# Kernel optimization log

Hardware: AMD Instinct MI355X
Metric: run time of the kernel (lower is better)

Reference implementation:

```python
import jax, jax.numpy as jnp
import numpy as np


def _mlp2(x, W1, b1, W2, b2):
    # ReluMLP with two Dense layers: relu between layers, linear output
    return jax.nn.relu(x @ W1 + b1) @ W2 + b2


def setup_inputs() -> dict:
    key = jax.random.key(0)
    N, NP, DIN, D = 100000, 25000, 16, 64
    E, EDS, EP, EUS = 1_600_000, 800_000, 400_000, 200_000
    L = 8  # number of message-passing layers actually used
    ks = iter(jax.random.split(key, 40))
    nrm = lambda shape: jax.random.normal(next(ks), shape, jnp.float32) * 0.05
    ri = lambda n, hi: jax.random.randint(next(ks), (n,), 0, hi)
    return dict(
        x=jax.random.normal(next(ks), (N, DIN), jnp.float32),
        We1=nrm((DIN, D)), be1=jnp.zeros((D,), jnp.float32),
        We2=nrm((D, D)), be2=jnp.zeros((D,), jnp.float32),
        Wm1=nrm((L, D, D)), bm1=jnp.zeros((L, D), jnp.float32),
        Wm2=nrm((L, D, D)), bm2=jnp.zeros((L, D), jnp.float32),
        Wn1=nrm((L, 2 * D, D)), bn1=jnp.zeros((L, D), jnp.float32),
        Wn2=nrm((L, D, D)), bn2=jnp.zeros((L, D), jnp.float32),
        Wd1=nrm((D, D)), bd1=jnp.zeros((D,), jnp.float32),
        Wd2=nrm((D, 2)), bd2=jnp.zeros((2,), jnp.float32),
        s_fine=ri(E, N), r_fine=ri(E, N),
        s_ds=ri(EDS, N), r_ds=ri(EDS, N),
        s_p=ri(EP, NP), r_p=ri(EP, NP),
        s_us=ri(EUS, NP), r_us=ri(EUS, NP),
        uppool=ri(N, NP), downpool=ri(NP, NP),
    )


def reference(x, We1, be1, We2, be2, Wm1, bm1, Wm2, bm2, Wn1, bn1, Wn2, bn2,
              Wd1, bd1, Wd2, bd2, s_fine, r_fine, s_ds, r_ds, s_p, r_p,
              s_us, r_us, uppool, downpool):
    def mp(l, h, s, r, n):
        # LinearMessagePassingLayer: message MLP on sender feats,
        # sum-scatter to receivers (mean_aggr=False), node MLP on [h, aggr]
        msg = _mlp2(h[s], Wm1[l], bm1[l], Wm2[l], bm2[l])          # [E, D]
        aggr = jax.ops.segment_sum(msg, r, num_segments=n)          # [n, D]
        return _mlp2(jnp.concatenate([h, aggr], -1),
                     Wn1[l], bn1[l], Wn2[l], bn2[l])                # [n, D]

    N = x.shape[0]
    NP = downpool.shape[0]
    # encode
    h = _mlp2(x, We1, be1, We2, be2)                                 # [N, D]
    h = mp(0, h, s_fine, r_fine, N)
    h = mp(1, h, s_fine, r_fine, N)
    skip = h
    # Downsample: gather by uppool idx, MP on downsampling graph, select pooled
    g = mp(2, h[uppool], s_ds, r_ds, N)                              # [N, D]
    hp = g[downpool]                                                 # [NP, D]
    # bottleneck
    hp = mp(3, hp, s_p, r_p, NP)
    hp = mp(4, hp, s_p, r_p, NP)
    # Upsample: gather by downpool idx, MP on upsampling graph, select by uppool
    g = mp(5, hp[downpool], s_us, r_us, NP)                          # [NP, D]
    h = g[uppool]                                                    # [N, D]
    # decode with skip connections
    h = mp(6, h, s_fine, r_fine, N) + skip
    h = mp(7, h, s_fine, r_fine, N) + skip
    return _mlp2(h, Wd1, bd1, Wd2, bd2)                              # [N, 2]
```

## Files before the change

kernel.cpp:

```cpp
#include <hip/hip_runtime.h>

#define WG 256

#define MLP_FMA16(ACC, A, W) do { \
    ACC[0][0]=fmaf(A.x,W.x,ACC[0][0]); ACC[0][1]=fmaf(A.x,W.y,ACC[0][1]); \
    ACC[0][2]=fmaf(A.x,W.z,ACC[0][2]); ACC[0][3]=fmaf(A.x,W.w,ACC[0][3]); \
    ACC[1][0]=fmaf(A.y,W.x,ACC[1][0]); ACC[1][1]=fmaf(A.y,W.y,ACC[1][1]); \
    ACC[1][2]=fmaf(A.y,W.z,ACC[1][2]); ACC[1][3]=fmaf(A.y,W.w,ACC[1][3]); \
    ACC[2][0]=fmaf(A.z,W.x,ACC[2][0]); ACC[2][1]=fmaf(A.z,W.y,ACC[2][1]); \
    ACC[2][2]=fmaf(A.z,W.z,ACC[2][2]); ACC[2][3]=fmaf(A.z,W.w,ACC[2][3]); \
    ACC[3][0]=fmaf(A.w,W.x,ACC[3][0]); ACC[3][1]=fmaf(A.w,W.y,ACC[3][1]); \
    ACC[3][2]=fmaf(A.w,W.z,ACC[3][2]); ACC[3][3]=fmaf(A.w,W.w,ACC[3][3]); \
} while (0)

__device__ __forceinline__ void fill_role(int xcd, int w,
    const int* __restrict__ s, const int* __restrict__ r,
    int* __restrict__ cur, int* __restrict__ sl,
    int cap, int E, int n, int W)
{
    const int lo = (int)(((long)n * xcd) >> 3);
    const int hi = (int)(((long)n * (xcd + 1)) >> 3);
    int chunk = (E + W - 1) / W;
    chunk = (chunk + 3) & ~3;
    const int e0 = w * chunk;
    const int e1 = min(E, e0 + chunk);

    auto fill1 = [&](int v, int e) {
        if (v >= lo && v < hi) {
            const int sv = s[e];
            const int p = atomicAdd(&cur[v], 1);
            if (p < cap) sl[(size_t)v * cap + p] = sv;
        }
    };

    for (int e = e0 + (int)threadIdx.x * 4; e < e1; e += WG * 4) {
        if (e + 4 <= e1) {
            const int4 rv = *(const int4*)&r[e];
            fill1(rv.x, e + 0);
            fill1(rv.y, e + 1);
            fill1(rv.z, e + 2);
            fill1(rv.w, e + 3);
        } else {
            for (int j = 0; e + j < e1; ++j) fill1(r[e + j], e + j);
        }
    }
}

struct FillPair {
    const int* s0; const int* r0; int* cur0; int* sl0; int cap0, E0, n0, W0;
    const int* s1; const int* r1; int* cur1; int* sl1; int cap1, E1, n1, W1;
    int FILLB;
};

template<int DINA, bool HAS_B, bool HAS_SKIP, bool GATHER_A,
         int MSG_DOUT, bool PARTIAL_MSG, bool WRITE_OUT1>
__global__ __launch_bounds__(WG)
void mlp2_fused(const float* __restrict__ inA, const int* __restrict__ gidxA,
                const float* __restrict__ inB,
                const float* __restrict__ W1, const float* __restrict__ b1,
                const float* __restrict__ W2, const float* __restrict__ b2,
                const float* __restrict__ skip, float* __restrict__ out1,
                const float* __restrict__ M1, const float* __restrict__ mb1,
                const float* __restrict__ M2, const float* __restrict__ mb2,
                float* __restrict__ outM, int msgN, int n, FillPair fa)
{
    if (fa.FILLB > 0 && (int)blockIdx.x < fa.FILLB) {
        const int xcd = blockIdx.x & 7;
        const int w = blockIdx.x >> 3;
        if (w < fa.W0)
            fill_role(xcd, w, fa.s0, fa.r0, fa.cur0, fa.sl0, fa.cap0, fa.E0, fa.n0, fa.W0);
        else
            fill_role(xcd, w - fa.W0, fa.s1, fa.r1, fa.cur1, fa.sl1, fa.cap1, fa.E1, fa.n1, fa.W1);
        return;
    }
    const int bid = blockIdx.x - fa.FILLB;

    constexpr int XP = 68;
    __shared__ __align__(16) float sXT[64][XP];
    __shared__ __align__(16) float sW[64 * 64];
    __shared__ float sb[128];
    __shared__ float sW2d[128];
    __shared__ float sb2d[2];

    const int tid = threadIdx.x;
    const int tx = tid & 15, ty = tid >> 4;
    const int c0 = tx * 4, r0 = ty * 4;
    const int row0 = bid * 64;
    const int lrow = tid & 63;
    const int kq0 = (tid >> 6) * 4;

    for (int i = tid * 4; i < DINA * 64; i += WG * 4)
        *(float4*)&sW[i] = *(const float4*)&W1[i];
    if (tid < 64) sb[tid] = b1[tid];
    else if (tid < 128) sb[tid] = b2[tid - 64];

    {
        const int rg = min(row0 + lrow, n - 1);
        const int ra = GATHER_A ? gidxA[rg] : rg;
        const float* pA = inA + (size_t)ra * DINA;
        #pragma unroll
        for (int kq = kq0; kq < DINA; kq += 16) {
            const float4 v = *(const float4*)(pA + kq);
            sXT[kq + 0][lrow] = v.x; sXT[kq + 1][lrow] = v.y;
            sXT[kq + 2][lrow] = v.z; sXT[kq + 3][lrow] = v.w;
        }
    }
    __syncthreads();

    float acc[4][4] = {};
    #pragma unroll 8
    for (int k = 0; k < DINA; ++k) {
        const float4 a = *(const float4*)&sXT[k][r0];
        const float4 w = *(const float4*)&sW[k * 64 + c0];
        MLP_FMA16(acc, a, w);
    }

    if constexpr (HAS_B) {
        __syncthreads();
        for (int i = tid * 4; i < 64 * 64; i += WG * 4)
            *(float4*)&sW[i] = *(const float4*)&W1[DINA * 64 + i];
        {
            const int rg = min(row0 + lrow, n - 1);
            const float* pB = inB + (size_t)rg * 64;
            #pragma unroll
            for (int kq = kq0; kq < 64; kq += 16) {
                const float4 v = *(const float4*)(pB + kq);
                sXT[kq + 0][lrow] = v.x; sXT[kq + 1][lrow] = v.y;
                sXT[kq + 2][lrow] = v.z; sXT[kq + 3][lrow] = v.w;
            }
        }
        __syncthreads();
        #pragma unroll 8
        for (int k = 0; k < 64; ++k) {
            const float4 a = *(const float4*)&sXT[k][r0];
            const float4 w = *(const float4*)&sW[k * 64 + c0];
            MLP_FMA16(acc, a, w);
        }
    }
    __syncthreads();

    for (int i = tid * 4; i < 64 * 64; i += WG * 4)
        *(float4*)&sW[i] = *(const float4*)&W2[i];
    #pragma unroll
    for (int j = 0; j < 4; ++j) {
        const float bj = sb[c0 + j];
        *(float4*)&sXT[c0 + j][r0] = make_float4(
            fmaxf(acc[0][j] + bj, 0.f), fmaxf(acc[1][j] + bj, 0.f),
            fmaxf(acc[2][j] + bj, 0.f), fmaxf(acc[3][j] + bj, 0.f));
    }
    __syncthreads();

    float acc2[4][4] = {};
    #pragma unroll 8
    for (int k = 0; k < 64; ++k) {
        const float4 a = *(const float4*)&sXT[k][r0];
        const float4 w = *(const float4*)&sW[k * 64 + c0];
        MLP_FMA16(acc2, a, w);
    }

    float ofull[4][4];
    #pragma unroll
    for (int i = 0; i < 4; ++i) {
        const int row = row0 + r0 + i;
        float4 s = make_float4(0.f, 0.f, 0.f, 0.f);
        if (HAS_SKIP && row < n) s = *(const float4*)&skip[(size_t)row * 64 + c0];
        ofull[i][0] = acc2[i][0] + sb[64 + c0 + 0] + s.x;
        ofull[i][1] = acc2[i][1] + sb[64 + c0 + 1] + s.y;
        ofull[i][2] = acc2[i][2] + sb[64 + c0 + 2] + s.z;
        ofull[i][3] = acc2[i][3] + sb[64 + c0 + 3] + s.w;
        if (WRITE_OUT1 && row < n)
            *(float4*)&out1[(size_t)row * 64 + c0] =
                make_float4(ofull[i][0], ofull[i][1], ofull[i][2], ofull[i][3]);
    }

    if constexpr (MSG_DOUT > 0) {
        if (!PARTIAL_MSG || row0 < msgN) {
            __syncthreads();
            for (int i = tid * 4; i < 64 * 64; i += WG * 4)
                *(float4*)&sW[i] = *(const float4*)&M1[i];
            if constexpr (MSG_DOUT == 64) {
                if (tid < 64) sb[tid] = mb1[tid];
                else if (tid < 128) sb[tid] = mb2[tid - 64];
            } else {
                if (tid < 64) sb[tid] = mb1[tid];
                else if (tid < 192) sW2d[tid - 64] = M2[tid - 64];
                else if (tid < 194) sb2d[tid - 192] = mb2[tid - 192];
            }
            #pragma unroll
            for (int j = 0; j < 4; ++j)
                *(float4*)&sXT[c0 + j][r0] =
                    make_float4(ofull[0][j], ofull[1][j], ofull[2][j], ofull[3][j]);
            __syncthreads();

            float acc3[4][4] = {};
            #pragma unroll 8
            for (int k = 0; k < 64; ++k) {
                const float4 a = *(const float4*)&sXT[k][r0];
                const float4 w = *(const float4*)&sW[k * 64 + c0];
                MLP_FMA16(acc3, a, w);
            }
            __syncthreads();
            if constexpr (MSG_DOUT == 64) {
                for (int i = tid * 4; i < 64 * 64; i += WG * 4)
                    *(float4*)&sW[i] = *(const float4*)&M2[i];
            }
            #pragma unroll
            for (int j = 0; j < 4; ++j) {
                const float bj = sb[c0 + j];
                *(float4*)&sXT[c0 + j][r0] = make_float4(
                    fmaxf(acc3[0][j] + bj, 0.f), fmaxf(acc3[1][j] + bj, 0.f),
                    fmaxf(acc3[2][j] + bj, 0.f), fmaxf(acc3[3][j] + bj, 0.f));
            }
            __syncthreads();

            if constexpr (MSG_DOUT == 64) {
                float accM[4][4] = {};
                #pragma unroll 8
                for (int k = 0; k < 64; ++k) {
                    const float4 a = *(const float4*)&sXT[k][r0];
                    const float4 w = *(const float4*)&sW[k * 64 + c0];
                    MLP_FMA16(accM, a, w);
                }
                #pragma unroll
                for (int i = 0; i < 4; ++i) {
                    const int row = row0 + r0 + i;
                    if (row < msgN)
                        *(float4*)&outM[(size_t)row * 64 + c0] =
                            make_float4(accM[i][0] + sb[64 + c0 + 0],
                                        accM[i][1] + sb[64 + c0 + 1],
                                        accM[i][2] + sb[64 + c0 + 2],
                                        accM[i][3] + sb[64 + c0 + 3]);
                }
            } else {
                if (tid < 128) {
                    const int lr = tid >> 1, col = tid & 1;
                    float o0 = sb2d[col], o1 = 0.0f;
                    #pragma unroll 8
                    for (int k = 0; k < 64; k += 2) {
                        o0 = fmaf(sXT[k][lr],     sW2d[k * 2 + col],       o0);
                        o1 = fmaf(sXT[k + 1][lr], sW2d[(k + 1) * 2 + col], o1);
                    }
                    const int row = row0 + lr;
                    if (row < msgN) outM[(size_t)row * 2 + col] = o0 + o1;
                }
            }
        }
    }
}

template<int DINA, bool HAS_B, bool HAS_SKIP, bool GATHER_A>
__global__ __launch_bounds__(WG)
void mlp2_rt(const float* __restrict__ inA, const int* __restrict__ gidxA,
             const float* __restrict__ inB,
             const float* __restrict__ W1, const float* __restrict__ b1,
             const float* __restrict__ W2, const float* __restrict__ b2,
             const float* __restrict__ skip,
             float* __restrict__ out, int n)
{
    constexpr int XP = 68;
    __shared__ __align__(16) float sXT[64][XP];
    __shared__ __align__(16) float sW[64 * 64];
    __shared__ float sb[128];

    const int tid = threadIdx.x;
    const int tx = tid & 15, ty = tid >> 4;
    const int c0 = tx * 4, r0 = ty * 4;
    const int row0 = blockIdx.x * 64;
    const int lrow = tid & 63;
    const int kq0 = (tid >> 6) * 4;

    for (int i = tid * 4; i < DINA * 64; i += WG * 4)
        *(float4*)&sW[i] = *(const float4*)&W1[i];
    if (tid < 64) sb[tid] = b1[tid];
    else if (tid < 128) sb[tid] = b2[tid - 64];

    {
        const int rg = min(row0 + lrow, n - 1);
        const int ra = GATHER_A ? gidxA[rg] : rg;
        const float* pA = inA + (size_t)ra * DINA;
        #pragma unroll
        for (int kq = kq0; kq < DINA; kq += 16) {
            const float4 v = *(const float4*)(pA + kq);
            sXT[kq + 0][lrow] = v.x; sXT[kq + 1][lrow] = v.y;
            sXT[kq + 2][lrow] = v.z; sXT[kq + 3][lrow] = v.w;
        }
    }
    __syncthreads();

    float acc[4][4] = {};
    #pragma unroll 8
    for (int k = 0; k < DINA; ++k) {
        const float4 a = *(const float4*)&sXT[k][r0];
        const float4 w = *(const float4*)&sW[k * 64 + c0];
        MLP_FMA16(acc, a, w);
    }
    if constexpr (HAS_B) {
        __syncthreads();
        for (int i = tid * 4; i < 64 * 64; i += WG * 4)
            *(float4*)&sW[i] = *(const float4*)&W1[DINA * 64 + i];
        {
            const int rg = min(row0 + lrow, n - 1);
            const float* pB = inB + (size_t)rg * 64;
            #pragma unroll
            for (int kq = kq0; kq < 64; kq += 16) {
                const float4 v = *(const float4*)(pB + kq);
                sXT[kq + 0][lrow] = v.x; sXT[kq + 1][lrow] = v.y;
                sXT[kq + 2][lrow] = v.z; sXT[kq + 3][lrow] = v.w;
            }
        }
        __syncthreads();
        #pragma unroll 8
        for (int k = 0; k < 64; ++k) {
            const float4 a = *(const float4*)&sXT[k][r0];
            const float4 w = *(const float4*)&sW[k * 64 + c0];
            MLP_FMA16(acc, a, w);
        }
    }
    __syncthreads();

    for (int i = tid * 4; i < 64 * 64; i += WG * 4)
        *(float4*)&sW[i] = *(const float4*)&W2[i];
    #pragma unroll
    for (int j = 0; j < 4; ++j) {
        const float bj = sb[c0 + j];
        *(float4*)&sXT[c0 + j][r0] = make_float4(
            fmaxf(acc[0][j] + bj, 0.f), fmaxf(acc[1][j] + bj, 0.f),
            fmaxf(acc[2][j] + bj, 0.f), fmaxf(acc[3][j] + bj, 0.f));
    }
    __syncthreads();

    float acc2[4][4] = {};
    #pragma unroll 8
    for (int k = 0; k < 64; ++k) {
        const float4 a = *(const float4*)&sXT[k][r0];
        const float4 w = *(const float4*)&sW[k * 64 + c0];
        MLP_FMA16(acc2, a, w);
    }
    #pragma unroll
    for (int i = 0; i < 4; ++i) {
        const int row = row0 + r0 + i;
        if (row < n) {
            float4 o = make_float4(acc2[i][0] + sb[64 + c0 + 0],
                                   acc2[i][1] + sb[64 + c0 + 1],
                                   acc2[i][2] + sb[64 + c0 + 2],
                                   acc2[i][3] + sb[64 + c0 + 3]);
            if (HAS_SKIP) {
                const float4 s = *(const float4*)&skip[(size_t)row * 64 + c0];
                o.x += s.x; o.y += s.y; o.z += s.z; o.w += s.w;
            }
            *(float4*)&out[(size_t)row * 64 + c0] = o;
        }
    }
}

__global__ __launch_bounds__(WG)
void fill_enc_k(const int* __restrict__ s0, const int* __restrict__ r0v,
                int* cu0, int* sl0, int cap0, int E0, int n0, int W0, int FILLB,
                const float* __restrict__ x,
                const float* __restrict__ We1, const float* __restrict__ be1,
                const float* __restrict__ We2, const float* __restrict__ be2,
                float* __restrict__ h0,
                const float* __restrict__ M1, const float* __restrict__ mb1,
                const float* __restrict__ M2, const float* __restrict__ mb2,
                float* __restrict__ msg0, int N)
{
    constexpr int XP = 68;
    __shared__ __align__(16) float sXT[64][XP];
    __shared__ float sb[128];

    if ((int)blockIdx.x < FILLB) {
        fill_role(blockIdx.x & 7, blockIdx.x >> 3, s0, r0v, cu0, sl0, cap0, E0, n0, W0);
        return;
    }

    const int bid = blockIdx.x - FILLB;
    const int tid = threadIdx.x;
    const int tx = tid & 15, ty = tid >> 4;
    const int c0 = tx * 4, r0 = ty * 4;
    const int row0 = bid * 64;
    const int lrow = tid & 63;
    const int kq0 = (tid >> 6) * 4;

    if (tid < 64) sb[tid] = be1[tid];
    else if (tid < 128) sb[tid] = be2[tid - 64];

    {
        const int rg = min(row0 + lrow, N - 1);
        const float* pA = x + (size_t)rg * 16;
        const float4 v = *(const float4*)(pA + kq0);
        sXT[kq0 + 0][lrow] = v.x; sXT[kq0 + 1][lrow] = v.y;
        sXT[kq0 + 2][lrow] = v.z; sXT[kq0 + 3][lrow] = v.w;
    }
    __syncthreads();

    float acc[4][4] = {};
    #pragma unroll
    for (int k = 0; k < 16; ++k) {
        const float4 a = *(const float4*)&sXT[k][r0];
        const float4 w = *(const float4*)&We1[k * 64 + c0];
        MLP_FMA16(acc, a, w);
    }
    __syncthreads();
    #pragma unroll
    for (int j = 0; j < 4; ++j) {
        const float bj = sb[c0 + j];
        *(float4*)&sXT[c0 + j][r0] = make_float4(
            fmaxf(acc[0][j] + bj, 0.f), fmaxf(acc[1][j] + bj, 0.f),
            fmaxf(acc[2][j] + bj, 0.f), fmaxf(acc[3][j] + bj, 0.f));
    }
    __syncthreads();

    float acc2[4][4] = {};
    #pragma unroll 8
    for (int k = 0; k < 64; ++k) {
        const float4 a = *(const float4*)&sXT[k][r0];
        const float4 w = *(const float4*)&We2[k * 64 + c0];
        MLP_FMA16(acc2, a, w);
    }
    float ofull[4][4];
    #pragma unroll
    for (int i = 0; i < 4; ++i) {
        const int row = row0 + r0 + i;
        ofull[i][0] = acc2[i][0] + sb[64 + c0 + 0];
        ofull[i][1] = acc2[i][1] + sb[64 + c0 + 1];
        ofull[i][2] = acc2[i][2] + sb[64 + c0 + 2];
        ofull[i][3] = acc2[i][3] + sb[64 + c0 + 3];
        if (row < N)
            *(float4*)&h0[(size_t)row * 64 + c0] =
                make_float4(ofull[i][0], ofull[i][1], ofull[i][2], ofull[i][3]);
    }

    __syncthreads();
    if (tid < 64) sb[tid] = mb1[tid];
    else if (tid < 128) sb[tid] = mb2[tid - 64];
    #pragma unroll
    for (int j = 0; j < 4; ++j)
        *(float4*)&sXT[c0 + j][r0] =
            make_float4(ofull[0][j], ofull[1][j], ofull[2][j], ofull[3][j]);
    __syncthreads();

    float acc3[4][4] = {};
    #pragma unroll 8
    for (int k = 0; k < 64; ++k) {
        const float4 a = *(const float4*)&sXT[k][r0];
        const float4 w = *(const float4*)&M1[k * 64 + c0];
        MLP_FMA16(acc3, a, w);
    }
    __syncthreads();
    #pragma unroll
    for (int j = 0; j < 4; ++j) {
        const float bj = sb[c0 + j];
        *(float4*)&sXT[c0 + j][r0] = make_float4(
            fmaxf(acc3[0][j] + bj, 0.f), fmaxf(acc3[1][j] + bj, 0.f),
            fmaxf(acc3[2][j] + bj, 0.f), fmaxf(acc3[3][j] + bj, 0.f));
    }
    __syncthreads();

    float accM[4][4] = {};
    #pragma unroll 8
    for (int k = 0; k < 64; ++k) {
        const float4 a = *(const float4*)&sXT[k][r0];
        const float4 w = *(const float4*)&M2[k * 64 + c0];
        MLP_FMA16(accM, a, w);
    }
    #pragma unroll
    for (int i = 0; i < 4; ++i) {
        const int row = row0 + r0 + i;
        if (row < N)
            *(float4*)&msg0[(size_t)row * 64 + c0] =
                make_float4(accM[i][0] + sb[64 + c0 + 0],
                            accM[i][1] + sb[64 + c0 + 1],
                            accM[i][2] + sb[64 + c0 + 2],
                            accM[i][3] + sb[64 + c0 + 3]);
    }
}

template<bool REMAP>
__global__ __launch_bounds__(WG)
void gather_slots_k(const int* __restrict__ deg, const int* __restrict__ slots,
                    int cap, const int* __restrict__ remap,
                    const float* __restrict__ tab, float* __restrict__ aggr, int n)
{
    const int node = blockIdx.x * (WG / 64) + (threadIdx.x >> 6);
    const int c = threadIdx.x & 63;
    if (node >= n) return;
    const int d = min(deg[node], cap);
    const int* sl = slots + (size_t)node * cap;

    int myidx = 0;
    if (c < d) {
        myidx = sl[c];
        if (REMAP) myidx = remap[myidx];
    }

    float a[8] = {};
    int j = 0;
    for (; j + 7 < d; j += 8) {
        #pragma unroll
        for (int u = 0; u < 8; ++u) {
            const int t = __shfl(myidx, j + u);
            a[u] += tab[(size_t)t * 64 + c];
        }
    }
    #pragma unroll 4
    for (; j < d; ++j) {
        const int t = __shfl(myidx, j);
        a[j & 7] += tab[(size_t)t * 64 + c];
    }
    aggr[(size_t)node * 64 + c] =
        ((a[0] + a[1]) + (a[2] + a[3])) + ((a[4] + a[5]) + (a[6] + a[7]));
}

extern "C" void kernel_launch(void* const* d_in, const int* in_sizes, int n_in,
                              void* d_out, int out_size, void* d_ws, size_t ws_size,
                              hipStream_t stream)
{
    const float* x    = (const float*)d_in[0];
    const float* We1  = (const float*)d_in[1];
    const float* be1  = (const float*)d_in[2];
    const float* We2  = (const float*)d_in[3];
    const float* be2  = (const float*)d_in[4];
    const float* Wm1  = (const float*)d_in[5];
    const float* bm1  = (const float*)d_in[6];
    const float* Wm2  = (const float*)d_in[7];
    const float* bm2  = (const float*)d_in[8];
    const float* Wn1  = (const float*)d_in[9];
    const float* bn1  = (const float*)d_in[10];
    const float* Wn2  = (const float*)d_in[11];
    const float* bn2  = (const float*)d_in[12];
    const float* Wd1  = (const float*)d_in[13];
    const float* bd1  = (const float*)d_in[14];
    const float* Wd2  = (const float*)d_in[15];
    const float* bd2  = (const float*)d_in[16];
    const int* s_fine = (const int*)d_in[17];
    const int* r_fine = (const int*)d_in[18];
    const int* s_ds   = (const int*)d_in[19];
    const int* r_ds   = (const int*)d_in[20];
    const int* s_p    = (const int*)d_in[21];
    const int* r_p    = (const int*)d_in[22];
    const int* s_us   = (const int*)d_in[23];
    const int* r_us   = (const int*)d_in[24];
    const int* uppool   = (const int*)d_in[25];
    const int* downpool = (const int*)d_in[26];

    const int N   = in_sizes[0] / 16;
    const int E   = in_sizes[17];
    const int EDS = in_sizes[19];
    const int EP  = in_sizes[21];
    const int EUS = in_sizes[23];
    const int NP  = in_sizes[26];

    const int CAP_FINE = 48, CAP_DS = 32, CAP_PP = 48, CAP_US = 32;

    float* B0  = (float*)d_ws;
    float* B1  = B0 + (size_t)N * 64;
    float* B2  = B1 + (size_t)N * 64;
    float* B3  = B2 + (size_t)N * 64;
    float* HPa = B3 + (size_t)N * 64;
    float* HPb = HPa + (size_t)NP * 64;
    int* ip = (int*)(HPb + (size_t)NP * 64);
    auto alloc_i = [&](size_t n) { int* p = ip; ip += n; return p; };
    int* cur_fine = alloc_i(N);
    int* cur_ds   = alloc_i(N);
    int* cur_pp   = alloc_i(NP);
    int* cur_us   = alloc_i(NP);
    int* sl_fine  = alloc_i((size_t)N * CAP_FINE);
    int* sl_ds    = alloc_i((size_t)N * CAP_DS);
    int* sl_pp    = alloc_i((size_t)NP * CAP_PP);
    int* sl_us    = alloc_i((size_t)NP * CAP_US);

    const int gN  = (N + 63) / 64;
    const int gNP = (NP + 63) / 64;
    const int gaN  = (N + 3) / 4;
    const int gaNP = (NP + 3) / 4;

    const FillPair fnone = {};

    hipMemsetAsync(cur_fine, 0, (size_t)(2 * N + 2 * NP) * sizeof(int), stream);
    {
        const int W_FINE = 256;
        const int FILLB = 8 * W_FINE;
        fill_enc_k<<<FILLB + gN, WG, 0, stream>>>(
            s_fine, r_fine, cur_fine, sl_fine, CAP_FINE, E, N, W_FINE, FILLB,
            x, We1, be1, We2, be2, B0,
            Wm1 + 0*4096, bm1 + 0*64, Wm2 + 0*4096, bm2 + 0*64, B1, N);
    }
    gather_slots_k<false><<<gaN,WG,0,stream>>>(cur_fine,sl_fine,CAP_FINE,nullptr,B1,B2,N);

    {
        const int W_DS = 128;
        FillPair fds = { s_ds, r_ds, cur_ds, sl_ds, CAP_DS, EDS, N, W_DS,
                         nullptr, nullptr, nullptr, nullptr, 0, 0, 0, 0,
                         8 * W_DS };
        mlp2_fused<64,true,false,false,64,false,true><<<8*W_DS + gN,WG,0,stream>>>(
            B0,nullptr,B2, Wn1+0*8192,bn1+0*64,Wn2+0*4096,bn2+0*64, nullptr,B3,
            Wm1+1*4096,bm1+1*64,Wm2+1*4096,bm2+1*64, B0, N, N, fds);
    }
    gather_slots_k<false><<<gaN,WG,0,stream>>>(cur_fine,sl_fine,CAP_FINE,nullptr,B0,B2,N);

    {
        const int W_PP = 64, W_US = 32;
        FillPair fpu = { s_p,  r_p,  cur_pp, sl_pp, CAP_PP, EP,  NP, W_PP,
                         s_us, r_us, cur_us, sl_us, CAP_US, EUS, NP, W_US,
                         8 * (W_PP + W_US) };
        mlp2_fused<64,true,false,false,64,true,true><<<8*(W_PP+W_US) + gN,WG,0,stream>>>(
            B3,nullptr,B2, Wn1+1*8192,bn1+1*64,Wn2+1*4096,bn2+1*64, nullptr,B1,
            Wm1+2*4096,bm1+2*64,Wm2+2*4096,bm2+2*64, B0, NP, N, fpu);
    }
    gather_slots_k<true><<<gaN,WG,0,stream>>>(cur_ds,sl_ds,CAP_DS,uppool,B0,B2,N);

    mlp2_rt<64,true,false,true><<<gN,WG,0,stream>>>(
        B1,uppool,B2, Wn1+2*8192,bn1+2*64,Wn2+2*4096,bn2+2*64, nullptr,B3,N);

    mlp2_rt<64,false,false,true><<<gNP,WG,0,stream>>>(
        B3,downpool,nullptr, Wm1+3*4096,bm1+3*64,Wm2+3*4096,bm2+3*64, nullptr,HPa,NP);
    gather_slots_k<false><<<gaNP,WG,0,stream>>>(cur_pp,sl_pp,CAP_PP,nullptr,HPa,B2,NP);

    mlp2_fused<64,true,false,true,64,false,true><<<gNP,WG,0,stream>>>(
        B3,downpool,B2, Wn1+3*8192,bn1+3*64,Wn2+3*4096,bn2+3*64, nullptr,HPb,
        Wm1+4*4096,bm1+4*64,Wm2+4*4096,bm2+4*64, HPa, NP, NP, fnone);
    gather_slots_k<false><<<gaNP,WG,0,stream>>>(cur_pp,sl_pp,CAP_PP,nullptr,HPa,B2,NP);

    mlp2_fused<64,true,false,false,64,false,true><<<gNP,WG,0,stream>>>(
        HPb,nullptr,B2, Wn1+4*8192,bn1+4*64,Wn2+4*4096,bn2+4*64, nullptr,HPa,
        Wm1+5*4096,bm1+5*64,Wm2+5*4096,bm2+5*64, HPb, NP, NP, fnone);
    gather_slots_k<true><<<gaNP,WG,0,stream>>>(cur_us,sl_us,CAP_US,downpool,HPb,B2,NP);

    mlp2_fused<64,true,false,true,64,false,true><<<gNP,WG,0,stream>>>(
        HPa,downpool,B2, Wn1+5*8192,bn1+5*64,Wn2+5*4096,bn2+5*64, nullptr,HPb,
        Wm1+6*4096,bm1+6*64,Wm2+6*4096,bm2+6*64, B3, NP, NP, fnone);
    gather_slots_k<true><<<gaN,WG,0,stream>>>(cur_fine,sl_fine,CAP_FINE,uppool,B3,B2,N);

    mlp2_fused<64,true,true,true,64,false,true><<<gN,WG,0,stream>>>(
        HPb,uppool,B2, Wn1+6*8192,bn1+6*64,Wn2+6*4096,bn2+6*64, B1,B0,
        Wm1+7*4096,bm1+7*64,Wm2+7*4096,bm2+7*64, B3, N, N, fnone);
    gather_slots_k<false><<<gaN,WG,0,stream>>>(cur_fine,sl_fine,CAP_FINE,nullptr,B3,B2,N);

    mlp2_fused<64,true,true,false,2,false,false><<<gN,WG,0,stream>>>(
        B0,nullptr,B2, Wn1+7*8192,bn1+7*64,Wn2+7*4096,bn2+7*64, B1,nullptr,
        Wd1,bd1,Wd2,bd2, (float*)d_out, N, N, fnone);
}
```

Before: 988.1 us.

## Fuse slot-based neighbor aggregation into node-MLP kernels, removing gather launches

Removes the standalone gather_slots_k kernels. The per-receiver sum over CSR-like slots now runs inside the node-MLP kernel and writes straight into shared memory. This avoids writing and re-reading the [n,64] aggregate buffer and cuts roughly eight launches. In exchange, each block's wavefronts walk 16 nodes serially, with variable degree inside the MLP kernel. That can hurt latency hiding and occupancy, and the layer-7 message MLP is split out into its own launch.

```diff
diff --git a/kernel.cpp b/kernel.cpp
--- a/kernel.cpp
+++ b/kernel.cpp
@@ -1,6 +1,7 @@
 #include <hip/hip_runtime.h>
 
 #define WG 256
+constexpr int XP = 68;
 
 #define MLP_FMA16(ACC, A, W) do { \
     ACC[0][0]=fmaf(A.x,W.x,ACC[0][0]); ACC[0][1]=fmaf(A.x,W.y,ACC[0][1]); \
@@ -52,17 +53,58 @@
     int FILLB;
 };
 
-template<int DINA, bool HAS_B, bool HAS_SKIP, bool GATHER_A,
+template<bool REMAP>
+__device__ __forceinline__ void gather_stage(
+    float (*sXT)[XP], int row0, int n,
+    const int* __restrict__ deg, const int* __restrict__ slots, int cap,
+    const int* __restrict__ remap, const float* __restrict__ tab, int tid)
+{
+    const int lane = tid & 63;
+    const int wv = tid >> 6;
+    #pragma unroll 1
+    for (int nn = 0; nn < 16; ++nn) {
+        const int ndl = wv * 16 + nn;
+        const int nd = row0 + ndl;
+        int d = 0;
+        const int* sl = slots;
+        if (nd < n) { d = min(deg[nd], cap); sl = slots + (size_t)nd * cap; }
+        int myidx = 0;
+        if (lane < d) {
+            myidx = sl[lane];
+            if (REMAP) myidx = remap[myidx];
+        }
+        float a[8] = {};
+        int j = 0;
+        for (; j + 7 < d; j += 8) {
+            #pragma unroll
+            for (int u = 0; u < 8; ++u) {
+                const int t = __shfl(myidx, j + u);
+                a[u] += tab[(size_t)t * 64 + lane];
+            }
+        }
+        #pragma unroll 4
+        for (; j < d; ++j) {
+            const int t = __shfl(myidx, j);
+            a[j & 7] += tab[(size_t)t * 64 + lane];
+        }
+        sXT[lane][ndl] =
+            ((a[0] + a[1]) + (a[2] + a[3])) + ((a[4] + a[5]) + (a[6] + a[7]));
+    }
+}
+
+template<int DINA, bool HAS_B, bool HAS_SKIP, bool GATHER_A, bool REMAP_B,
          int MSG_DOUT, bool PARTIAL_MSG, bool WRITE_OUT1>
 __global__ __launch_bounds__(WG)
 void mlp2_fused(const float* __restrict__ inA, const int* __restrict__ gidxA,
-                const float* __restrict__ inB,
                 const float* __restrict__ W1, const float* __restrict__ b1,
                 const float* __restrict__ W2, const float* __restrict__ b2,
                 const float* __restrict__ skip, float* __restrict__ out1,
                 const float* __restrict__ M1, const float* __restrict__ mb1,
                 const float* __restrict__ M2, const float* __restrict__ mb2,
-                float* __restrict__ outM, int msgN, int n, FillPair fa)
+                float* __restrict__ outM, int msgN, int n,
+                const int* __restrict__ degB, const int* __restrict__ slotsB,
+                int capB, const int* __restrict__ remapB,
+                const float* __restrict__ tabB, FillPair fa)
 {
     if (fa.FILLB > 0 && (int)blockIdx.x < fa.FILLB) {
         const int xcd = blockIdx.x & 7;
@@ -75,7 +117,6 @@
     }
     const int bid = blockIdx.x - fa.FILLB;
 
-    constexpr int XP = 68;
     __shared__ __align__(16) float sXT[64][XP];
     __shared__ __align__(16) float sW[64 * 64];
     __shared__ float sb[128];
@@ -119,16 +160,7 @@
         __syncthreads();
         for (int i = tid * 4; i < 64 * 64; i += WG * 4)
             *(float4*)&sW[i] = *(const float4*)&W1[DINA * 64 + i];
-        {
-            const int rg = min(row0 + lrow, n - 1);
-            const float* pB = inB + (size_t)rg * 64;
-            #pragma unroll
-            for (int kq = kq0; kq < 64; kq += 16) {
-                const float4 v = *(const float4*)(pB + kq);
-                sXT[kq + 0][lrow] = v.x; sXT[kq + 1][lrow] = v.y;
-                sXT[kq + 2][lrow] = v.z; sXT[kq + 3][lrow] = v.w;
-            }
-        }
+        gather_stage<REMAP_B>(sXT, row0, n, degB, slotsB, capB, remapB, tabB, tid);
         __syncthreads();
         #pragma unroll 8
         for (int k = 0; k < 64; ++k) {
@@ -248,111 +280,6 @@
     }
 }
 
-template<int DINA, bool HAS_B, bool HAS_SKIP, bool GATHER_A>
-__global__ __launch_bounds__(WG)
-void mlp2_rt(const float* __restrict__ inA, const int* __restrict__ gidxA,
-             const float* __restrict__ inB,
-             const float* __restrict__ W1, const float* __restrict__ b1,
-             const float* __restrict__ W2, const float* __restrict__ b2,
-             const float* __restrict__ skip,
-             float* __restrict__ out, int n)
-{
-    constexpr int XP = 68;
-    __shared__ __align__(16) float sXT[64][XP];
-    __shared__ __align__(16) float sW[64 * 64];
-    __shared__ float sb[128];
-
-    const int tid = threadIdx.x;
-    const int tx = tid & 15, ty = tid >> 4;
-    const int c0 = tx * 4, r0 = ty * 4;
-    const int row0 = blockIdx.x * 64;
-    const int lrow = tid & 63;
-    const int kq0 = (tid >> 6) * 4;
-
-    for (int i = tid * 4; i < DINA * 64; i += WG * 4)
-        *(float4*)&sW[i] = *(const float4*)&W1[i];
-    if (tid < 64) sb[tid] = b1[tid];
-    else if (tid < 128) sb[tid] = b2[tid - 64];
-
-    {
-        const int rg = min(row0 + lrow, n - 1);
-        const int ra = GATHER_A ? gidxA[rg] : rg;
-        const float* pA = inA + (size_t)ra * DINA;
-        #pragma unroll
-        for (int kq = kq0; kq < DINA; kq += 16) {
-            const float4 v = *(const float4*)(pA + kq);
-            sXT[kq + 0][lrow] = v.x; sXT[kq + 1][lrow] = v.y;
-            sXT[kq + 2][lrow] = v.z; sXT[kq + 3][lrow] = v.w;
-        }
-    }
-    __syncthreads();
-
-    float acc[4][4] = {};
-    #pragma unroll 8
-    for (int k = 0; k < DINA; ++k) {
-        const float4 a = *(const float4*)&sXT[k][r0];
-        const float4 w = *(const float4*)&sW[k * 64 + c0];
-        MLP_FMA16(acc, a, w);
-    }
-    if constexpr (HAS_B) {
-        __syncthreads();
-        for (int i = tid * 4; i < 64 * 64; i += WG * 4)
-            *(float4*)&sW[i] = *(const float4*)&W1[DINA * 64 + i];
-        {
-            const int rg = min(row0 + lrow, n - 1);
-            const float* pB = inB + (size_t)rg * 64;
-            #pragma unroll
-            for (int kq = kq0; kq < 64; kq += 16) {
-                const float4 v = *(const float4*)(pB + kq);
-                sXT[kq + 0][lrow] = v.x; sXT[kq + 1][lrow] = v.y;
-                sXT[kq + 2][lrow] = v.z; sXT[kq + 3][lrow] = v.w;
-            }
-        }
-        __syncthreads();
-        #pragma unroll 8
-        for (int k = 0; k < 64; ++k) {
-            const float4 a = *(const float4*)&sXT[k][r0];
-            const float4 w = *(const float4*)&sW[k * 64 + c0];
-            MLP_FMA16(acc, a, w);
-        }
-    }
-    __syncthreads();
-
-    for (int i = tid * 4; i < 64 * 64; i += WG * 4)
-        *(float4*)&sW[i] = *(const float4*)&W2[i];
-    #pragma unroll
-    for (int j = 0; j < 4; ++j) {
-        const float bj = sb[c0 + j];
-        *(float4*)&sXT[c0 + j][r0] = make_float4(
-            fmaxf(acc[0][j] + bj, 0.f), fmaxf(acc[1][j] + bj, 0.f),
-            fmaxf(acc[2][j] + bj, 0.f), fmaxf(acc[3][j] + bj, 0.f));
-    }
-    __syncthreads();
-
-    float acc2[4][4] = {};
-    #pragma unroll 8
-    for (int k = 0; k < 64; ++k) {
-        const float4 a = *(const float4*)&sXT[k][r0];
-        const float4 w = *(const float4*)&sW[k * 64 + c0];
-        MLP_FMA16(acc2, a, w);
-    }
-    #pragma unroll
-    for (int i = 0; i < 4; ++i) {
-        const int row = row0 + r0 + i;
-        if (row < n) {
-            float4 o = make_float4(acc2[i][0] + sb[64 + c0 + 0],
-                                   acc2[i][1] + sb[64 + c0 + 1],
-                                   acc2[i][2] + sb[64 + c0 + 2],
-                                   acc2[i][3] + sb[64 + c0 + 3]);
-            if (HAS_SKIP) {
-                const float4 s = *(const float4*)&skip[(size_t)row * 64 + c0];
-                o.x += s.x; o.y += s.y; o.z += s.z; o.w += s.w;
-            }
-            *(float4*)&out[(size_t)row * 64 + c0] = o;
-        }
-    }
-}
-
 __global__ __launch_bounds__(WG)
 void fill_enc_k(const int* __restrict__ s0, const int* __restrict__ r0v,
                 int* cu0, int* sl0, int cap0, int E0, int n0, int W0, int FILLB,
@@ -364,7 +291,6 @@
                 const float* __restrict__ M2, const float* __restrict__ mb2,
                 float* __restrict__ msg0, int N)
 {
-    constexpr int XP = 68;
     __shared__ __align__(16) float sXT[64][XP];
     __shared__ float sb[128];
 
@@ -473,42 +399,6 @@
                             accM[i][2] + sb[64 + c0 + 2],
                             accM[i][3] + sb[64 + c0 + 3]);
     }
-}
-
-template<bool REMAP>
-__global__ __launch_bounds__(WG)
-void gather_slots_k(const int* __restrict__ deg, const int* __restrict__ slots,
-                    int cap, const int* __restrict__ remap,
-                    const float* __restrict__ tab, float* __restrict__ aggr, int n)
-{
-    const int node = blockIdx.x * (WG / 64) + (threadIdx.x >> 6);
-    const int c = threadIdx.x & 63;
-    if (node >= n) return;
-    const int d = min(deg[node], cap);
-    const int* sl = slots + (size_t)node * cap;
-
-    int myidx = 0;
-    if (c < d) {
-        myidx = sl[c];
-        if (REMAP) myidx = remap[myidx];
-    }
-
-    float a[8] = {};
-    int j = 0;
-    for (; j + 7 < d; j += 8) {
-        #pragma unroll
-        for (int u = 0; u < 8; ++u) {
-            const int t = __shfl(myidx, j + u);
-            a[u] += tab[(size_t)t * 64 + c];
-        }
-    }
-    #pragma unroll 4
-    for (; j < d; ++j) {
-        const int t = __shfl(myidx, j);
-        a[j & 7] += tab[(size_t)t * 64 + c];
-    }
-    aggr[(size_t)node * 64 + c] =
-        ((a[0] + a[1]) + (a[2] + a[3])) + ((a[4] + a[5]) + (a[6] + a[7]));
 }
 
 extern "C" void kernel_launch(void* const* d_in, const int* in_sizes, int n_in,
@@ -571,8 +461,6 @@
 
     const int gN  = (N + 63) / 64;
     const int gNP = (NP + 63) / 64;
-    const int gaN  = (N + 3) / 4;
-    const int gaNP = (NP + 3) / 4;
 
     const FillPair fnone = {};
 
@@ -585,58 +473,66 @@
             x, We1, be1, We2, be2, B0,
             Wm1 + 0*4096, bm1 + 0*64, Wm2 + 0*4096, bm2 + 0*64, B1, N);
     }
-    gather_slots_k<false><<<gaN,WG,0,stream>>>(cur_fine,sl_fine,CAP_FINE,nullptr,B1,B2,N);
 
     {
         const int W_DS = 128;
         FillPair fds = { s_ds, r_ds, cur_ds, sl_ds, CAP_DS, EDS, N, W_DS,
                          nullptr, nullptr, nullptr, nullptr, 0, 0, 0, 0,
                          8 * W_DS };
-        mlp2_fused<64,true,false,false,64,false,true><<<8*W_DS + gN,WG,0,stream>>>(
-            B0,nullptr,B2, Wn1+0*8192,bn1+0*64,Wn2+0*4096,bn2+0*64, nullptr,B3,
-            Wm1+1*4096,bm1+1*64,Wm2+1*4096,bm2+1*64, B0, N, N, fds);
-    }
-    gather_slots_k<false><<<gaN,WG,0,stream>>>(cur_fine,sl_fine,CAP_FINE,nullptr,B0,B2,N);
+        mlp2_fused<64,true,false,false,false,64,false,true><<<8*W_DS + gN,WG,0,stream>>>(
+            B0,nullptr, Wn1+0*8192,bn1+0*64,Wn2+0*4096,bn2+0*64, nullptr,B2,
+            Wm1+1*4096,bm1+1*64,Wm2+1*4096,bm2+1*64, B3, N, N,
+            cur_fine, sl_fine, CAP_FINE, nullptr, B1, fds);
+    }
 
     {
         const int W_PP = 64, W_US = 32;
         FillPair fpu = { s_p,  r_p,  cur_pp, sl_pp, CAP_PP, EP,  NP, W_PP,
                          s_us, r_us, cur_us, sl_us, CAP_US, EUS, NP, W_US,
                          8 * (W_PP + W_US) };
-        mlp2_fused<64,true,false,false,64,true,true><<<8*(W_PP+W_US) + gN,WG,0,stream>>>(
-            B3,nullptr,B2, Wn1+1*8192,bn1+1*64,Wn2+1*4096,bn2+1*64, nullptr,B1,
-            Wm1+2*4096,bm1+2*64,Wm2+2*4096,bm2+2*64, B0, NP, N, fpu);
-    }
-    gather_slots_k<true><<<gaN,WG,0,stream>>>(cur_ds,sl_ds,CAP_DS,uppool,B0,B2,N);
-
-    mlp2_rt<64,true,false,true><<<gN,WG,0,stream>>>(
-        B1,uppool,B2, Wn1+2*8192,bn1+2*64,Wn2+2*4096,bn2+2*64, nullptr,B3,N);
-
-    mlp2_rt<64,false,false,true><<<gNP,WG,0,stream>>>(
-        B3,downpool,nullptr, Wm1+3*4096,bm1+3*64,Wm2+3*4096,bm2+3*64, nullptr,HPa,NP);
-    gather_slots_k<false><<<gaNP,WG,0,stream>>>(cur_pp,sl_pp,CAP_PP,nullptr,HPa,B2,NP);
-
-    mlp2_fused<64,true,false,true,64,false,true><<<gNP,WG,0,stream>>>(
-        B3,downpool,B2, Wn1+3*8192,bn1+3*64,Wn2+3*4096,bn2+3*64, nullptr,HPb,
-        Wm1+4*4096,bm1+4*64,Wm2+4*4096,bm2+4*64, HPa, NP, NP, fnone);
-    gather_slots_k<false><<<gaNP,WG,0,stream>>>(cur_pp,sl_pp,CAP_PP,nullptr,HPa,B2,NP);
-
-    mlp2_fused<64,true,false,false,64,false,true><<<gNP,WG,0,stream>>>(
-        HPb,nullptr,B2, Wn1+4*8192,bn1+4*64,Wn2+4*4096,bn2+4*64, nullptr,HPa,
-        Wm1+5*4096,bm1+5*64,Wm2+5*4096,bm2+5*64, HPb, NP, NP, fnone);
-    gather_slots_k<true><<<gaNP,WG,0,stream>>>(cur_us,sl_us,CAP_US,downpool,HPb,B2,NP);
-
-    mlp2_fused<64,true,false,true,64,false,true><<<gNP,WG,0,stream>>>(
-        HPa,downpool,B2, Wn1+5*8192,bn1+5*64,Wn2+5*4096,bn2+5*64, nullptr,HPb,
-        Wm1+6*4096,bm1+6*64,Wm2+6*4096,bm2+6*64, B3, NP, NP, fnone);
-    gather_slots_k<true><<<gaN,WG,0,stream>>>(cur_fine,sl_fine,CAP_FINE,uppool,B3,B2,N);
-
-    mlp2_fused<64,true,true,true,64,false,true><<<gN,WG,0,stream>>>(
-        HPb,uppool,B2, Wn1+6*8192,bn1+6*64,Wn2+6*4096,bn2+6*64, B1,B0,
-        Wm1+7*4096,bm1+7*64,Wm2+7*4096,bm2+7*64, B3, N, N, fnone);
-    gather_slots_k<false><<<gaN,WG,0,stream>>>(cur_fine,sl_fine,CAP_FINE,nullptr,B3,B2,N);
-
-    mlp2_fused<64,true,true,false,2,false,false><<<gN,WG,0,stream>>>(
-        B0,nullptr,B2, Wn1+7*8192,bn1+7*64,Wn2+7*4096,bn2+7*64, B1,nullptr,
-        Wd1,bd1,Wd2,bd2, (float*)d_out, N, N, fnone);
+        mlp2_fused<64,true,false,false,false,64,true,true><<<8*(W_PP+W_US) + gN,WG,0,stream>>>(
+            B2,nullptr, Wn1+1*8192,bn1+1*64,Wn2+1*4096,bn2+1*64, nullptr,B0,
+            Wm1+2*4096,bm1+2*64,Wm2+2*4096,bm2+2*64, B1, NP, N,
+            cur_fine, sl_fine, CAP_FINE, nullptr, B3, fpu);
+    }
+
+    mlp2_fused<64,true,false,true,true,0,false,true><<<gN,WG,0,stream>>>(
+        B0,uppool, Wn1+2*8192,bn1+2*64,Wn2+2*4096,bn2+2*64, nullptr,B2,
+        nullptr,nullptr,nullptr,nullptr, nullptr, 0, N,
+        cur_ds, sl_ds, CAP_DS, uppool, B1, fnone);
+
+    mlp2_fused<64,false,false,true,false,0,false,true><<<gNP,WG,0,stream>>>(
+        B2,downpool, Wm1+3*4096,bm1+3*64,Wm2+3*4096,bm2+3*64, nullptr,HPa,
+        nullptr,nullptr,nullptr,nullptr, nullptr, 0, NP,
+        nullptr, nullptr, 0, nullptr, nullptr, fnone);
+
+    mlp2_fused<64,true,false,true,false,64,false,true><<<gNP,WG,0,stream>>>(
+        B2,downpool, Wn1+3*8192,bn1+3*64,Wn2+3*4096,bn2+3*64, nullptr,HPb,
+        Wm1+4*4096,bm1+4*64,Wm2+4*4096,bm2+4*64, B1, NP, NP,
+        cur_pp, sl_pp, CAP_PP, nullptr, HPa, fnone);
+
+    mlp2_fused<64,true,false,false,false,64,false,true><<<gNP,WG,0,stream>>>(
+        HPb,nullptr, Wn1+4*8192,bn1+4*64,Wn2+4*4096,bn2+4*64, nullptr,HPa,
+        Wm1+5*4096,bm1+5*64,Wm2+5*4096,bm2+5*64, HPb, NP, NP,
+        cur_pp, sl_pp, CAP_PP, nullptr, B1, fnone);
+
+    mlp2_fused<64,true,false,true,true,64,false,true><<<gNP,WG,0,stream>>>(
+        HPa,downpool, Wn1+5*8192,bn1+5*64,Wn2+5*4096,bn2+5*64, nullptr,B1,
+        Wm1+6*4096,bm1+6*64,Wm2+6*4096,bm2+6*64, B3, NP, NP,
+        cur_us, sl_us, CAP_US, downpool, HPb, fnone);
+
+    mlp2_fused<64,true,true,true,true,0,false,true><<<gN,WG,0,stream>>>(
+        B1,uppool, Wn1+6*8192,bn1+6*64,Wn2+6*4096,bn2+6*64, B0,B2,
+        nullptr,nullptr,nullptr,nullptr, nullptr, 0, N,
+        cur_fine, sl_fine, CAP_FINE, uppool, B3, fnone);
+
+    mlp2_fused<64,false,false,false,false,0,false,true><<<gN,WG,0,stream>>>(
+        B2,nullptr, Wm1+7*4096,bm1+7*64,Wm2+7*4096,bm2+7*64, nullptr,B1,
+        nullptr,nullptr,nullptr,nullptr, nullptr, 0, N,
+        nullptr, nullptr, 0, nullptr, nullptr, fnone);
+
+    mlp2_fused<64,true,true,false,false,2,false,false><<<gN,WG,0,stream>>>(
+        B2,nullptr, Wn1+7*8192,bn1+7*64,Wn2+7*4096,bn2+7*64, B0,nullptr,
+        Wd1,bd1,Wd2,bd2, (float*)d_out, N, N,
+        cur_fine, sl_fine, CAP_FINE, nullptr, B1, fnone);
 }
```

Result: slower. 1.220 ms (+23.4%).
